# Performance work log

Hardware: AMD Instinct MI355X
Metric: run time of the kernel (lower is better)

Reference implementation:

```python
import jax, jax.numpy as jnp
import numpy as np

N_NODES = 100000
N_EDGES = 1600000
N_GRAPHS = 512


def gcn_conv(x, row, col, W, b):
    # x: [N, Cin], row/col: [E] (self-loops already appended)
    n = x.shape[0]
    h = x @ W                                        # [N, Cout]
    deg = jax.ops.segment_sum(jnp.ones_like(col, dtype=x.dtype), col, num_segments=n)
    dinv = jnp.where(deg > 0, deg ** -0.5, 0.0)
    norm = dinv[row] * dinv[col]                     # [E]
    msg = norm[:, None] * h[row]                     # [E, Cout]
    out = jax.ops.segment_sum(msg, col, num_segments=n)
    return out + b


def setup_inputs() -> dict:
    key = jax.random.key(0)
    ks = jax.random.split(key, 10)
    x = jax.random.normal(ks[0], (N_NODES, 128), dtype=jnp.float32)
    edge_index = jax.random.randint(ks[1], (2, N_EDGES), 0, N_NODES, dtype=jnp.int64)
    batch = jnp.sort(jax.random.randint(ks[2], (N_NODES,), 0, N_GRAPHS, dtype=jnp.int64))
    def lin_w(k, fan_in, fan_out):
        bound = 1.0 / np.sqrt(fan_in)
        return jax.random.uniform(k, (fan_in, fan_out), jnp.float32, -bound, bound)
    # GCN layers (bias zero-initialized per reset_parameters)
    W1 = lin_w(ks[3], 128, 128); b1 = jnp.zeros((128,), jnp.float32)
    W2 = lin_w(ks[4], 128, 128); b2 = jnp.zeros((128,), jnp.float32)
    # MLP layers (Linear with bias)
    Wm1 = lin_w(ks[5], 128, 64)
    bm1 = jax.random.uniform(ks[6], (64,), jnp.float32, -1/np.sqrt(128), 1/np.sqrt(128))
    Wm2 = lin_w(ks[7], 64, 1)
    bm2 = jax.random.uniform(ks[8], (1,), jnp.float32, -1/np.sqrt(64), 1/np.sqrt(64))
    return {"x": x, "edge_index": edge_index, "batch": batch,
            "W1": W1, "b1": b1, "W2": W2, "b2": b2,
            "Wm1": Wm1, "bm1": bm1, "Wm2": Wm2, "bm2": bm2}


def reference(x, edge_index, batch, W1, b1, W2, b2, Wm1, bm1, Wm2, bm2):
    n = x.shape[0]
    loops = jnp.arange(n, dtype=edge_index.dtype)
    row = jnp.concatenate([edge_index[0], loops])
    col = jnp.concatenate([edge_index[1], loops])
    # GCN: conv -> relu -> conv
    h = gcn_conv(x, row, col, W1, b1)
    h = jax.nn.relu(h)
    h = gcn_conv(h, row, col, W2, b2)
    # scatter-mean pooling over graphs
    sums = jax.ops.segment_sum(h, batch, num_segments=N_GRAPHS)      # [G, C]
    counts = jax.ops.segment_sum(jnp.ones((n,), h.dtype), batch, num_segments=N_GRAPHS)
    g = sums / jnp.maximum(counts, 1.0)[:, None]
    # MLP: linear -> relu -> linear
    g = jax.nn.relu(g @ Wm1 + bm1)
    out = g @ Wm2 + bm2
    return out
```

## Files before the change

### kernel.cpp

```cpp
#include <hip/hip_runtime.h>
#include <math.h>

#define C_DIM 128
#define POOL_CHUNK 64
#define BKT_SHIFT 7
#define MAX_B 1024
#define CB 256
typedef unsigned short ushort_t;
typedef __attribute__((ext_vector_type(8))) short short8;
typedef __attribute__((ext_vector_type(4))) float f32x4;

static inline int ceil_div(int a, int b) { return (a + b - 1) / b; }

__device__ inline ushort_t f2bf(float f) {
    union { float f; unsigned u; } v; v.f = f;
    unsigned r = v.u + 0x7FFFu + ((v.u >> 16) & 1u);
    return (ushort_t)(r >> 16);
}
__device__ inline float bf2f(unsigned s) {
    union { unsigned u; float f; } v; v.u = s << 16; return v.f;
}


__global__ __launch_bounds__(256) void k_bcount(
    const int* __restrict__ col, int E, int chunk, int B,
    int* __restrict__ counts) {
    __shared__ int hist[MAX_B];
    int t = threadIdx.x;
    for (int i = t; i < B; i += 256) hist[i] = 0;
    __syncthreads();
    int s = blockIdx.x * chunk;
    int e = s + chunk; if (e > E) e = E;
    for (int i = s + t; i < e; i += 256)
        atomicAdd(&hist[col[i] >> BKT_SHIFT], 1);
    __syncthreads();
    for (int i = t; i < B; i += 256)
        counts[(size_t)i * CB + blockIdx.x] = hist[i];
}

__global__ __launch_bounds__(256) void k_bscan(
    int* __restrict__ counts, int* __restrict__ btot) {
    __shared__ int sd[256];
    int b = blockIdx.x, t = threadIdx.x;
    int v = counts[(size_t)b * CB + t];
    sd[t] = v;
    __syncthreads();
    for (int off = 1; off < 256; off <<= 1) {
        int x = (t >= off) ? sd[t - off] : 0;
        __syncthreads();
        sd[t] += x;
        __syncthreads();
    }
    counts[(size_t)b * CB + t] = sd[t] - v;
    if (t == 255) btot[b] = sd[255];
}

__global__ __launch_bounds__(256) void k_btotscan(
    const int* __restrict__ btot, int* __restrict__ bbase, int B, int E,
    int* __restrict__ offs, int N) {
    __shared__ int sd[256];
    __shared__ int carry_s;
    int t = threadIdx.x;
    if (t == 0) carry_s = 0;
    __syncthreads();
    int nc = (B + 255) / 256;
    for (int c = 0; c < nc; ++c) {
        int idx = c * 256 + t;
        int v = (idx < B) ? btot[idx] : 0;
        sd[t] = v;
        __syncthreads();
        for (int off = 1; off < 256; off <<= 1) {
            int x = (t >= off) ? sd[t - off] : 0;
            __syncthreads();
            sd[t] += x;
            __syncthreads();
        }
        int pre = sd[t] - v + carry_s;
        if (idx < B) bbase[idx] = pre;
        __syncthreads();
        if (t == 0) carry_s += sd[255];
        __syncthreads();
    }
    if (t == 0) { bbase[B] = E; offs[N] = E; }
}

__global__ __launch_bounds__(256) void k_bscatter(
    const int* __restrict__ row, const int* __restrict__ col, int E, int chunk,
    int B, const int* __restrict__ counts, const int* __restrict__ bbase,
    int2* __restrict__ epk) {
    __shared__ int cur[MAX_B];
    int t = threadIdx.x, blk = blockIdx.x;
    for (int i = t; i < B; i += 256)
        cur[i] = bbase[i] + counts[(size_t)i * CB + blk];
    __syncthreads();
    int s = blk * chunk;
    int e = s + chunk; if (e > E) e = E;
    for (int i = s + t; i < e; i += 256) {
        int c = col[i];
        int r = row[i];
        int slot = atomicAdd(&cur[c >> BKT_SHIFT], 1);
        epk[slot] = make_int2(r, c);
    }
}

__global__ __launch_bounds__(256) void k_bfinal(
    const int2* __restrict__ epk, const int* __restrict__ bbase, int N,
    int* __restrict__ offs, float* __restrict__ dinv, int* __restrict__ csr) {
    __shared__ int cnt[128];
    __shared__ int pre[128];
    __shared__ int cur[128];
    int bkt = blockIdx.x, t = threadIdx.x;
    int s = bbase[bkt], e = bbase[bkt + 1];
    int base = bkt << BKT_SHIFT;
    int nn = N - base; if (nn > 128) nn = 128;
    if (t < 128) cnt[t] = 0;
    __syncthreads();
    for (int i = s + t; i < e; i += 256)
        atomicAdd(&cnt[epk[i].y & 127], 1);
    __syncthreads();
    if (t < 128) pre[t] = cnt[t];
    __syncthreads();
    for (int off = 1; off < 128; off <<= 1) {
        int x = (t >= off && t < 128) ? pre[t - off] : 0;
        __syncthreads();
        if (t < 128) pre[t] += x;
        __syncthreads();
    }
    if (t < 128) {
        int ex = pre[t] - cnt[t];
        cur[t] = ex;
        if (t < nn) {
            offs[base + t] = s + ex;
            dinv[base + t] = 1.0f / sqrtf((float)cnt[t] + 1.0f);
        }
    }
    __syncthreads();
    for (int i = s + t; i < e; i += 256) {
        int2 rc = epk[i];
        int slot = atomicAdd(&cur[rc.y & 127], 1);
        csr[s + slot] = rc.x;
    }
}

__global__ __launch_bounds__(256) void k_wfrag(
    const float* __restrict__ W, uint4* __restrict__ wf) {
    int t = threadIdx.x;
    for (int f = t; f < 2048; f += 256) {
        int lane = f & 63, kkn = f >> 6;
        int kk = kkn & 3, nt = kkn >> 2;
        int n = lane & 15, quad = lane >> 4;
        union { ushort_t h[8]; uint4 v; } u;
#pragma unroll
        for (int j = 0; j < 8; ++j)
            u.h[j] = f2bf(W[(size_t)(kk * 32 + quad * 8 + j) * C_DIM + nt * 16 + n]);
        wf[f] = u.v;
    }
}

template <int ABF16>
__global__ __launch_bounds__(256) void k_matmul_mfma(
    const float* __restrict__ Af, const ushort_t* __restrict__ Abf,
    const uint4* __restrict__ wfrag, const float* __restrict__ dinv,
    ushort_t* __restrict__ Cb, int N) {
    __shared__ __align__(16) ushort_t eb[64 * 136];
    int t = threadIdx.x;
    int wv = t >> 6, lane = t & 63;
    int n = lane & 15, quad = lane >> 4;
    int row0 = blockIdx.x * 64;
    int rowA = row0 + wv * 16 + n;
    int rowAc = rowA < N ? rowA : N - 1;

    f32x4 acc[8];
#pragma unroll
    for (int i = 0; i < 8; ++i) acc[i] = (f32x4){0.f, 0.f, 0.f, 0.f};

#pragma unroll
    for (int kk = 0; kk < 4; ++kk) {
        short8 a;
        if (ABF16) {
            uint4 u = *(const uint4*)(Abf + (size_t)rowAc * C_DIM + kk * 32 + quad * 8);
            union { uint4 v; short8 s; } c; c.v = u;
            a = c.s;
        } else {
            const float4* ap = (const float4*)(Af + (size_t)rowAc * C_DIM + kk * 32 + quad * 8);
            float4 f0 = ap[0], f1 = ap[1];
            union { ushort_t h[8]; short8 s; } c;
            c.h[0] = f2bf(f0.x); c.h[1] = f2bf(f0.y); c.h[2] = f2bf(f0.z); c.h[3] = f2bf(f0.w);
            c.h[4] = f2bf(f1.x); c.h[5] = f2bf(f1.y); c.h[6] = f2bf(f1.z); c.h[7] = f2bf(f1.w);
            a = c.s;
        }
#pragma unroll
        for (int nt = 0; nt < 8; ++nt) {
            uint4 bu = wfrag[(nt * 4 + kk) * 64 + lane];
            union { uint4 v; short8 s; } c; c.v = bu;
            acc[nt] = __builtin_amdgcn_mfma_f32_16x16x32_bf16(a, c.s, acc[nt], 0, 0, 0);
        }
    }

#pragma unroll
    for (int reg = 0; reg < 4; ++reg) {
        int rl = wv * 16 + quad * 4 + reg;
        int r = row0 + rl;
        float s = dinv[r < N ? r : N - 1];
#pragma unroll
        for (int nt = 0; nt < 8; ++nt)
            eb[rl * 136 + nt * 16 + n] = f2bf(acc[nt][reg] * s);
    }
    __syncthreads();
    int rows = N - row0; if (rows > 64) rows = 64;
    for (int idx = t; idx < 16 * 64; idx += 256) {
        int r = idx >> 4, c8 = idx & 15;
        if (r < rows)
            *(uint4*)(Cb + (size_t)(row0 + r) * C_DIM + c8 * 8) =
                *(const uint4*)&eb[r * 136 + c8 * 8];
    }
}

template <int RELU>
__global__ __launch_bounds__(256) void k_aggregate(
    const ushort_t* __restrict__ hs, const int* __restrict__ offs,
    const int* __restrict__ csr, const float* __restrict__ dinv,
    const float* __restrict__ bias, unsigned* __restrict__ outU, int N) {
    int node = (blockIdx.x << 2) + (threadIdx.x >> 6);
    if (node >= N) return;
    int t = threadIdx.x & 63;
    int s = offs[node], e = offs[node + 1];
    float ax, ay;
    {
        unsigned u = ((const unsigned*)(hs + (size_t)node * C_DIM))[t];
        ax = bf2f(u & 0xFFFFu); ay = bf2f(u >> 16);
    }
    int j = s;
    for (; j + 8 <= e; j += 8) {
        int r[8];
#pragma unroll
        for (int k = 0; k < 8; ++k) r[k] = csr[j + k];
        unsigned u[8];
#pragma unroll
        for (int k = 0; k < 8; ++k)
            u[k] = ((const unsigned*)(hs + (size_t)r[k] * C_DIM))[t];
#pragma unroll
        for (int k = 0; k < 8; ++k) {
            ax += bf2f(u[k] & 0xFFFFu);
            ay += bf2f(u[k] >> 16);
        }
    }
    for (; j + 2 <= e; j += 2) {
        int r0 = csr[j], r1 = csr[j + 1];
        unsigned u0 = ((const unsigned*)(hs + (size_t)r0 * C_DIM))[t];
        unsigned u1 = ((const unsigned*)(hs + (size_t)r1 * C_DIM))[t];
        ax += bf2f(u0 & 0xFFFFu) + bf2f(u1 & 0xFFFFu);
        ay += bf2f(u0 >> 16) + bf2f(u1 >> 16);
    }
    if (j < e) {
        unsigned u = ((const unsigned*)(hs + (size_t)csr[j] * C_DIM))[t];
        ax += bf2f(u & 0xFFFFu); ay += bf2f(u >> 16);
    }
    float dn = dinv[node];
    float ox = dn * ax + bias[2 * t];
    float oy = dn * ay + bias[2 * t + 1];
    if (RELU) { ox = fmaxf(ox, 0.f); oy = fmaxf(oy, 0.f); }
    outU[(size_t)node * 64 + t] = (unsigned)f2bf(ox) | ((unsigned)f2bf(oy) << 16);
}

__global__ __launch_bounds__(128) void k_pool_sum(
    const ushort_t* __restrict__ h, const int* __restrict__ batch, int n,
    float* __restrict__ sums) {
    int r0 = blockIdx.x * POOL_CHUNK;
    int r1 = r0 + POOL_CHUNK; if (r1 > n) r1 = n;
    if (r0 >= n) return;
    int t = threadIdx.x;
    int g = batch[r0];
    float run = 0.f;
    int i = r0;
    while (i < r1) {
        if (i + 4 <= r1 && batch[i + 3] == g) {
            float a0 = bf2f(h[(size_t)i * C_DIM + t]);
            float a1 = bf2f(h[(size_t)(i + 1) * C_DIM + t]);
            float a2 = bf2f(h[(size_t)(i + 2) * C_DIM + t]);
            float a3 = bf2f(h[(size_t)(i + 3) * C_DIM + t]);
            run += (a0 + a1) + (a2 + a3);
            i += 4;
        } else {
            int bi = batch[i];
            if (bi != g) { atomicAdd(&sums[(size_t)g * C_DIM + t], run); run = 0.f; g = bi; }
            run += bf2f(h[(size_t)i * C_DIM + t]);
            ++i;
        }
    }
    atomicAdd(&sums[(size_t)g * C_DIM + t], run);
}

__global__ __launch_bounds__(128) void k_mlp(
    const float* __restrict__ sums, const int* __restrict__ batch, int n,
    const float* __restrict__ Wm1, const float* __restrict__ bm1,
    const float* __restrict__ Wm2, const float* __restrict__ bm2,
    float* __restrict__ out) {
    int g = blockIdx.x;
    int t = threadIdx.x;
    int lo = 0, hi = n;
    while (lo < hi) { int m = (lo + hi) >> 1; if (batch[m] < g) lo = m + 1; else hi = m; }
    int start = lo;
    lo = start; hi = n;
    while (lo < hi) { int m = (lo + hi) >> 1; if (batch[m] < g + 1) lo = m + 1; else hi = m; }
    float cnt = (float)(lo - start);

    float mean = sums[(size_t)g * C_DIM + t] / fmaxf(cnt, 1.0f);

    __shared__ float m_s[128];
    __shared__ float hid[64];
    m_s[t] = mean;
    __syncthreads();
    if (t < 64) {
        float a = bm1[t];
#pragma unroll 4
        for (int k = 0; k < 128; ++k) a += m_s[k] * Wm1[k * 64 + t];
        hid[t] = fmaxf(a, 0.f) * Wm2[t];
    }
    __syncthreads();
    if (t < 64) {
        float v = hid[t];
        for (int off = 32; off > 0; off >>= 1) v += __shfl_down(v, off);
        if (t == 0) out[g] = v + bm2[0];
    }
}

extern "C" void kernel_launch(void* const* d_in, const int* in_sizes, int n_in,
                              void* d_out, int out_size, void* d_ws, size_t ws_size,
                              hipStream_t stream) {
    const float* x     = (const float*)d_in[0];
    const int*   eidx  = (const int*)d_in[1];
    const int*   batch = (const int*)d_in[2];
    const float* W1    = (const float*)d_in[3];
    const float* b1    = (const float*)d_in[4];
    const float* W2    = (const float*)d_in[5];
    const float* b2    = (const float*)d_in[6];
    const float* Wm1   = (const float*)d_in[7];
    const float* bm1   = (const float*)d_in[8];
    const float* Wm2   = (const float*)d_in[9];
    const float* bm2   = (const float*)d_in[10];

    const int N = in_sizes[2];
    const int E = in_sizes[1] / 2;
    const int G = out_size;
    const int B = (N + 127) >> BKT_SHIFT;

    char* p = (char*)d_ws;
    auto carve = [&](size_t bytes) {
        char* q = p;
        p += (bytes + 255) & ~(size_t)255;
        return q;
    };
    ushort_t* bufT   = (ushort_t*)carve((size_t)N * C_DIM * sizeof(ushort_t));
    ushort_t* bufA   = (ushort_t*)carve((size_t)N * C_DIM * sizeof(ushort_t));
    float*    dinv   = (float*)   carve((size_t)N * sizeof(float));
    int*      offs   = (int*)     carve((size_t)(N + 1) * sizeof(int));
    int*      csr    = (int*)     carve((size_t)E * sizeof(int));
    int*      counts = (int*)     carve((size_t)B * CB * sizeof(int));
    int*      btot   = (int*)     carve((size_t)B * sizeof(int));
    int*      bbase  = (int*)     carve((size_t)(B + 1) * sizeof(int));
    float*    gsums  = (float*)   carve((size_t)G * C_DIM * sizeof(float));
    uint4*    wf1    = (uint4*)   carve(2048 * sizeof(uint4));
    uint4*    wf2    = (uint4*)   carve(2048 * sizeof(uint4));
    int2*     epk    = (int2*)bufT;

    const int* erow = eidx;
    const int* ecol = eidx + E;
    const int chunk = ceil_div(E, CB);

    hipMemsetAsync(gsums, 0, (size_t)G * C_DIM * sizeof(float), stream);

    k_bcount<<<CB, 256, 0, stream>>>(ecol, E, chunk, B, counts);
    k_bscan<<<B, 256, 0, stream>>>(counts, btot);
    k_btotscan<<<1, 256, 0, stream>>>(btot, bbase, B, E, offs, N);
    k_bscatter<<<CB, 256, 0, stream>>>(erow, ecol, E, chunk, B, counts, bbase, epk);
    k_bfinal<<<B, 256, 0, stream>>>(epk, bbase, N, offs, dinv, csr);

    k_wfrag<<<1, 256, 0, stream>>>(W1, wf1);
    k_wfrag<<<1, 256, 0, stream>>>(W2, wf2);

    k_matmul_mfma<0><<<ceil_div(N, 64), 256, 0, stream>>>(x, nullptr, wf1, dinv, bufT, N);
    k_aggregate<1><<<ceil_div(N, 4), 256, 0, stream>>>(bufT, offs, csr, dinv, b1,
                                                       (unsigned*)bufA, N);
    k_matmul_mfma<1><<<ceil_div(N, 64), 256, 0, stream>>>(nullptr, bufA, wf2, dinv, bufT, N);
    k_aggregate<0><<<ceil_div(N, 4), 256, 0, stream>>>(bufT, offs, csr, dinv, b2,
                                                       (unsigned*)bufA, N);
    k_pool_sum<<<ceil_div(N, POOL_CHUNK), 128, 0, stream>>>(bufA, batch, N, gsums);
    k_mlp<<<G, 128, 0, stream>>>(gsums, batch, N, Wm1, bm1, Wm2, bm2, (float*)d_out);
}
```

Measured before the change: 346.4 us.

## Split aggregate wavefront into four edge lanes with 16-byte gathers and vectorize bucket passes

The aggregation kernel now splits each 64-lane wavefront into four groups of 16 lanes. Each group processes a different edge and loads a full 256-byte row as 16-byte vectors, and the partial sums are combined with cross-lane shuffles. This is meant to raise memory-level parallelism and cut instruction count per gathered byte in the dominant gather-reduce kernels. The bucket count and scatter kernels also read col/row as int4, with the chunk size rounded to a multiple of 4. That rounding assumes E is a multiple of 4 and that the edge arrays are 16-byte aligned; otherwise the last vector loads could read past the end.

Result: no change. 340.4 us (-1.7%).

```diff
diff --git a/kernel.cpp b/kernel.cpp
--- a/kernel.cpp
+++ b/kernel.cpp
@@ -20,6 +20,18 @@
 __device__ inline float bf2f(unsigned s) {
     union { unsigned u; float f; } v; v.u = s << 16; return v.f;
 }
+__device__ inline float bf_lo(unsigned u) {
+    union { unsigned v; float f; } c; c.v = u << 16; return c.f;
+}
+__device__ inline float bf_hi(unsigned u) {
+    union { unsigned v; float f; } c; c.v = u & 0xFFFF0000u; return c.f;
+}
+__device__ inline void accum8(uint4 u, float acc[8]) {
+    acc[0] += bf_lo(u.x); acc[1] += bf_hi(u.x);
+    acc[2] += bf_lo(u.y); acc[3] += bf_hi(u.y);
+    acc[4] += bf_lo(u.z); acc[5] += bf_hi(u.z);
+    acc[6] += bf_lo(u.w); acc[7] += bf_hi(u.w);
+}
 
 
 __global__ __launch_bounds__(256) void k_bcount(
@@ -31,8 +43,13 @@
     __syncthreads();
     int s = blockIdx.x * chunk;
     int e = s + chunk; if (e > E) e = E;
-    for (int i = s + t; i < e; i += 256)
-        atomicAdd(&hist[col[i] >> BKT_SHIFT], 1);
+    for (int i = s + 4 * t; i < e; i += 1024) {
+        int4 c = *(const int4*)(col + i);
+        atomicAdd(&hist[c.x >> BKT_SHIFT], 1);
+        atomicAdd(&hist[c.y >> BKT_SHIFT], 1);
+        atomicAdd(&hist[c.z >> BKT_SHIFT], 1);
+        atomicAdd(&hist[c.w >> BKT_SHIFT], 1);
+    }
     __syncthreads();
     for (int i = t; i < B; i += 256)
         counts[(size_t)i * CB + blockIdx.x] = hist[i];
@@ -95,11 +112,13 @@
     __syncthreads();
     int s = blk * chunk;
     int e = s + chunk; if (e > E) e = E;
-    for (int i = s + t; i < e; i += 256) {
-        int c = col[i];
-        int r = row[i];
-        int slot = atomicAdd(&cur[c >> BKT_SHIFT], 1);
-        epk[slot] = make_int2(r, c);
+    for (int i = s + 4 * t; i < e; i += 1024) {
+        int4 c = *(const int4*)(col + i);
+        int4 r = *(const int4*)(row + i);
+        int s0 = atomicAdd(&cur[c.x >> BKT_SHIFT], 1); epk[s0] = make_int2(r.x, c.x);
+        int s1 = atomicAdd(&cur[c.y >> BKT_SHIFT], 1); epk[s1] = make_int2(r.y, c.y);
+        int s2 = atomicAdd(&cur[c.z >> BKT_SHIFT], 1); epk[s2] = make_int2(r.z, c.z);
+        int s3 = atomicAdd(&cur[c.w >> BKT_SHIFT], 1); epk[s3] = make_int2(r.w, c.w);
     }
 }
 
@@ -220,47 +239,75 @@
 __global__ __launch_bounds__(256) void k_aggregate(
     const ushort_t* __restrict__ hs, const int* __restrict__ offs,
     const int* __restrict__ csr, const float* __restrict__ dinv,
-    const float* __restrict__ bias, unsigned* __restrict__ outU, int N) {
+    const float* __restrict__ bias, uint4* __restrict__ outV, int N) {
     int node = (blockIdx.x << 2) + (threadIdx.x >> 6);
     if (node >= N) return;
     int t = threadIdx.x & 63;
+    int q = t >> 4;
+    int fs = t & 15;
     int s = offs[node], e = offs[node + 1];
-    float ax, ay;
+
+    float acc[8];
     {
-        unsigned u = ((const unsigned*)(hs + (size_t)node * C_DIM))[t];
-        ax = bf2f(u & 0xFFFFu); ay = bf2f(u >> 16);
-    }
+        uint4 u = *(const uint4*)(hs + (size_t)node * C_DIM + fs * 8);
+        float v[8];
+        v[0] = bf_lo(u.x); v[1] = bf_hi(u.x);
+        v[2] = bf_lo(u.y); v[3] = bf_hi(u.y);
+        v[4] = bf_lo(u.z); v[5] = bf_hi(u.z);
+        v[6] = bf_lo(u.w); v[7] = bf_hi(u.w);
+#pragma unroll
+        for (int i = 0; i < 8; ++i) acc[i] = (q == 0) ? v[i] : 0.f;
+    }
+
     int j = s;
-    for (; j + 8 <= e; j += 8) {
-        int r[8];
-#pragma unroll
-        for (int k = 0; k < 8; ++k) r[k] = csr[j + k];
-        unsigned u[8];
-#pragma unroll
-        for (int k = 0; k < 8; ++k)
-            u[k] = ((const unsigned*)(hs + (size_t)r[k] * C_DIM))[t];
-#pragma unroll
-        for (int k = 0; k < 8; ++k) {
-            ax += bf2f(u[k] & 0xFFFFu);
-            ay += bf2f(u[k] >> 16);
-        }
-    }
-    for (; j + 2 <= e; j += 2) {
-        int r0 = csr[j], r1 = csr[j + 1];
-        unsigned u0 = ((const unsigned*)(hs + (size_t)r0 * C_DIM))[t];
-        unsigned u1 = ((const unsigned*)(hs + (size_t)r1 * C_DIM))[t];
-        ax += bf2f(u0 & 0xFFFFu) + bf2f(u1 & 0xFFFFu);
-        ay += bf2f(u0 >> 16) + bf2f(u1 >> 16);
-    }
-    if (j < e) {
-        unsigned u = ((const unsigned*)(hs + (size_t)csr[j] * C_DIM))[t];
-        ax += bf2f(u & 0xFFFFu); ay += bf2f(u >> 16);
-    }
-    float dn = dinv[node];
-    float ox = dn * ax + bias[2 * t];
-    float oy = dn * ay + bias[2 * t + 1];
-    if (RELU) { ox = fmaxf(ox, 0.f); oy = fmaxf(oy, 0.f); }
-    outU[(size_t)node * 64 + t] = (unsigned)f2bf(ox) | ((unsigned)f2bf(oy) << 16);
+    for (; j + 16 <= e; j += 16) {
+        int r[4];
+#pragma unroll
+        for (int b = 0; b < 4; ++b) r[b] = csr[j + b * 4 + q];
+        uint4 u[4];
+#pragma unroll
+        for (int b = 0; b < 4; ++b)
+            u[b] = *(const uint4*)(hs + (size_t)r[b] * C_DIM + fs * 8);
+#pragma unroll
+        for (int b = 0; b < 4; ++b) accum8(u[b], acc);
+    }
+    for (; j + 4 <= e; j += 4) {
+        int r = csr[j + q];
+        uint4 u = *(const uint4*)(hs + (size_t)r * C_DIM + fs * 8);
+        accum8(u, acc);
+    }
+    if (j + q < e) {
+        int r = csr[j + q];
+        uint4 u = *(const uint4*)(hs + (size_t)r * C_DIM + fs * 8);
+        accum8(u, acc);
+    }
+
+#pragma unroll
+    for (int i = 0; i < 8; ++i) {
+        acc[i] += __shfl_xor(acc[i], 16);
+        acc[i] += __shfl_xor(acc[i], 32);
+    }
+
+    if (q == 0) {
+        float dn = dinv[node];
+        float4 b0 = *(const float4*)(bias + fs * 8);
+        float4 b1 = *(const float4*)(bias + fs * 8 + 4);
+        float o[8];
+        o[0] = dn * acc[0] + b0.x; o[1] = dn * acc[1] + b0.y;
+        o[2] = dn * acc[2] + b0.z; o[3] = dn * acc[3] + b0.w;
+        o[4] = dn * acc[4] + b1.x; o[5] = dn * acc[5] + b1.y;
+        o[6] = dn * acc[6] + b1.z; o[7] = dn * acc[7] + b1.w;
+        if (RELU) {
+#pragma unroll
+            for (int i = 0; i < 8; ++i) o[i] = fmaxf(o[i], 0.f);
+        }
+        uint4 pk;
+        pk.x = (unsigned)f2bf(o[0]) | ((unsigned)f2bf(o[1]) << 16);
+        pk.y = (unsigned)f2bf(o[2]) | ((unsigned)f2bf(o[3]) << 16);
+        pk.z = (unsigned)f2bf(o[4]) | ((unsigned)f2bf(o[5]) << 16);
+        pk.w = (unsigned)f2bf(o[6]) | ((unsigned)f2bf(o[7]) << 16);
+        outV[(size_t)node * 16 + fs] = pk;
+    }
 }
 
 __global__ __launch_bounds__(128) void k_pool_sum(
@@ -366,7 +413,7 @@
 
     const int* erow = eidx;
     const int* ecol = eidx + E;
-    const int chunk = ceil_div(E, CB);
+    const int chunk = (ceil_div(E, CB) + 3) & ~3;
 
     hipMemsetAsync(gsums, 0, (size_t)G * C_DIM * sizeof(float), stream);
 
@@ -381,10 +428,10 @@
 
     k_matmul_mfma<0><<<ceil_div(N, 64), 256, 0, stream>>>(x, nullptr, wf1, dinv, bufT, N);
     k_aggregate<1><<<ceil_div(N, 4), 256, 0, stream>>>(bufT, offs, csr, dinv, b1,
-                                                       (unsigned*)bufA, N);
+                                                       (uint4*)bufA, N);
     k_matmul_mfma<1><<<ceil_div(N, 64), 256, 0, stream>>>(nullptr, bufA, wf2, dinv, bufT, N);
     k_aggregate<0><<<ceil_div(N, 4), 256, 0, stream>>>(bufT, offs, csr, dinv, b2,
-                                                       (unsigned*)bufA, N);
+                                                       (uint4*)bufA, N);
     k_pool_sum<<<ceil_div(N, POOL_CHUNK), 128, 0, stream>>>(bufA, batch, N, gsums);
     k_mlp<<<G, 128, 0, stream>>>(gsums, batch, N, Wm1, bm1, Wm2, bm2, (float*)d_out);
 }
```
